# Performance work log

Measured on AMD Instinct MI355X. Metric: run time of the kernel, lower is better.

## Reference

```python
import jax, jax.numpy as jnp
import numpy as np

NUM_HEAD = 12
DIM_MODEL = 768
HEAD_DIM = DIM_MODEL // NUM_HEAD


def setup_inputs() -> dict:
    key = jax.random.key(0)
    ks = jax.random.split(key, 4)
    B, S, D = 2, 2048, DIM_MODEL
    scale = 1.0 / np.sqrt(D)
    return {
        "v1": jax.random.normal(ks[0], (B, S, D), dtype=jnp.float32),
        "v1_mask": jnp.zeros((B, 1, 1, S), dtype=jnp.float32),
        "Wq": jax.random.normal(ks[1], (D, D), dtype=jnp.float32) * scale,
        "bq": jnp.zeros((D,), dtype=jnp.float32),
        "Wk": jax.random.normal(ks[2], (D, D), dtype=jnp.float32) * scale,
        "bk": jnp.zeros((D,), dtype=jnp.float32),
        "Wv": jax.random.normal(ks[3], (D, D), dtype=jnp.float32) * scale,
        "bv": jnp.zeros((D,), dtype=jnp.float32),
    }


def reference(v1, v1_mask, Wq, bq, Wk, bk, Wv, bv):
    B, S, D = v1.shape
    H, hd = NUM_HEAD, HEAD_DIM

    def split_heads(x):  # [B,S,D] -> [B,H,S,hd]
        return x.reshape(B, S, H, hd).transpose(0, 2, 1, 3)

    q = split_heads(v1 @ Wq + bq)
    k = split_heads(v1 @ Wk + bk)
    v = split_heads(v1 @ Wv + bv)

    scores = jnp.einsum("bhqd,bhkd->bhqk", q, k) / jnp.sqrt(jnp.float32(hd))
    scores = scores + v1_mask  # additive mask broadcasts over heads/query
    probs = jax.nn.softmax(scores, axis=-1)
    # dropout is identity in eval/reference mode
    ctx = jnp.einsum("bhqk,bhkd->bhqd", probs, v)
    return ctx.transpose(0, 2, 1, 3).reshape(B, S, D)
```

## Files before the change

kernel.cpp:

```cpp
#include <hip/hip_runtime.h>
#include <math.h>

#define B_SZ 2
#define S_SZ 2048
#define D_SZ 768
#define NH   12
#define HD   64
#define BH_T (B_SZ * NH)
#define M_TOT (B_SZ * S_SZ)

using bfrag = __attribute__((ext_vector_type(8))) short;
using ffrag = __attribute__((ext_vector_type(4))) float;

__device__ __forceinline__ unsigned short f2bf(float f) {
    unsigned int u = __float_as_uint(f);
    u += 0x7fffu + ((u >> 16) & 1u);
    return (unsigned short)(u >> 16);
}
__device__ __forceinline__ unsigned short f2bf_fast(float f) {
    return (unsigned short)((__float_as_uint(f) + 0x8000u) >> 16);
}

__device__ __forceinline__ void async16(void* lds, const void* gp) {
    __builtin_amdgcn_global_load_lds(
        (const __attribute__((address_space(1))) unsigned int*)gp,
        (__attribute__((address_space(3))) unsigned int*)lds,
        16, 0, 0);
}

__global__ __launch_bounds__(256) void cvt_v1(const float* __restrict__ in,
                                              unsigned short* __restrict__ out) {
    int i = (blockIdx.x * 256 + threadIdx.x) * 4;
    float4 v = *(const float4*)&in[i];
    ushort4 o;
    o.x = f2bf(v.x); o.y = f2bf(v.y); o.z = f2bf(v.z); o.w = f2bf(v.w);
    *(ushort4*)&out[i] = o;
}

__global__ __launch_bounds__(256) void transpose_w(
    const float* __restrict__ Wq, const float* __restrict__ Wk,
    const float* __restrict__ Wv, unsigned short* __restrict__ Wt) {
    const int z = blockIdx.z;
    const float* W = (z == 0) ? Wq : (z == 1) ? Wk : Wv;
    unsigned short* dst = Wt + (size_t)z * D_SZ * D_SZ;
    __shared__ float tile[64][65];
    const int t = threadIdx.x;
    const int n0 = blockIdx.x * 64, k0 = blockIdx.y * 64;
    #pragma unroll
    for (int i = 0; i < 16; ++i) {
        int flat = i * 256 + t;
        int r = flat >> 6, c = flat & 63;
        tile[r][c] = W[(size_t)(k0 + r) * D_SZ + n0 + c];
    }
    __syncthreads();
    #pragma unroll
    for (int i = 0; i < 16; ++i) {
        int flat = i * 256 + t;
        int r = flat >> 6, c = flat & 63;
        dst[(size_t)(n0 + r) * D_SZ + k0 + c] = f2bf(tile[c][r]);
    }
}

__global__ __launch_bounds__(256) void proj_gemm(
    const unsigned short* __restrict__ Ab,
    const unsigned short* __restrict__ Wt,
    const float* __restrict__ bq, const float* __restrict__ bk_,
    const float* __restrict__ bv_,
    unsigned short* __restrict__ Qb, unsigned short* __restrict__ Kb,
    unsigned short* __restrict__ Vtb) {
    const int z = blockIdx.z;
    const unsigned short* Bt = Wt + (size_t)z * D_SZ * D_SZ;
    const float* bias = (z == 0) ? bq : (z == 1) ? bk_ : bv_;

    __shared__ unsigned short As[128 * 64];
    __shared__ unsigned short Bs[128 * 64];

    const int t = threadIdx.x;
    const int lane = t & 63;
    const int w = t >> 6;
    const int wm = w & 1, wn = w >> 1;
    const int col = lane & 15;
    const int quad = lane >> 4;
    const int m0 = blockIdx.y * 128;
    const int n0 = blockIdx.x * 128;
    const int wbase = t & ~63;

    ffrag acc[4][4];
    #pragma unroll
    for (int i = 0; i < 4; ++i)
        #pragma unroll
        for (int j = 0; j < 4; ++j) { ffrag zf = {0.f, 0.f, 0.f, 0.f}; acc[i][j] = zf; }

    for (int k0 = 0; k0 < D_SZ; k0 += 64) {
        __syncthreads();
        #pragma unroll
        for (int i = 0; i < 4; ++i) {
            int c = i * 256 + t;
            int row = c >> 3;
            int gcol = ((c & 7) ^ (row & 7)) * 8;
            async16(&As[(size_t)(i * 256 + wbase) * 8],
                    &Ab[(size_t)(m0 + row) * D_SZ + k0 + gcol]);
        }
        #pragma unroll
        for (int i = 0; i < 4; ++i) {
            int c = i * 256 + t;
            int row = c >> 3;
            int gcol = ((c & 7) ^ (row & 7)) * 8;
            async16(&Bs[(size_t)(i * 256 + wbase) * 8],
                    &Bt[(size_t)(n0 + row) * D_SZ + k0 + gcol]);
        }
        __syncthreads();
        #pragma unroll
        for (int kk = 0; kk < 64; kk += 32) {
            const int cc = (kk >> 3) + quad;
            bfrag a[4], b[4];
            #pragma unroll
            for (int mi = 0; mi < 4; ++mi) {
                int row = wm * 64 + mi * 16 + col;
                a[mi] = *(const bfrag*)&As[row * 64 + ((cc ^ (row & 7)) * 8)];
            }
            #pragma unroll
            for (int ni = 0; ni < 4; ++ni) {
                int row = wn * 64 + ni * 16 + col;
                b[ni] = *(const bfrag*)&Bs[row * 64 + ((cc ^ (row & 7)) * 8)];
            }
            if (z == 2) {
                #pragma unroll
                for (int mi = 0; mi < 4; ++mi)
                    #pragma unroll
                    for (int ni = 0; ni < 4; ++ni)
                        acc[mi][ni] = __builtin_amdgcn_mfma_f32_16x16x32_bf16(
                            a[mi], b[ni], acc[mi][ni], 0, 0, 0);
            } else {
                #pragma unroll
                for (int mi = 0; mi < 4; ++mi)
                    #pragma unroll
                    for (int ni = 0; ni < 4; ++ni)
                        acc[mi][ni] = __builtin_amdgcn_mfma_f32_16x16x32_bf16(
                            b[ni], a[mi], acc[mi][ni], 0, 0, 0);
            }
        }
    }

    if (z < 2) {
        unsigned short* Out = (z == 0) ? Qb : Kb;
        const float sc = (z == 0) ? 0.125f : 1.0f;
        #pragma unroll
        for (int mi = 0; mi < 4; ++mi) {
            int m = m0 + wm * 64 + mi * 16 + col;
            int bb = m >> 11, s = m & 2047;
            #pragma unroll
            for (int ni = 0; ni < 4; ++ni) {
                int nb = n0 + wn * 64 + ni * 16 + quad * 4;
                int h = nb >> 6, d = nb & 63;
                float4 b4 = *(const float4*)&bias[nb];
                float v0 = (acc[mi][ni][0] + b4.x) * sc;
                float v1 = (acc[mi][ni][1] + b4.y) * sc;
                float v2 = (acc[mi][ni][2] + b4.z) * sc;
                float v3 = (acc[mi][ni][3] + b4.w) * sc;
                uint2 pk;
                pk.x = (unsigned)f2bf(v0) | ((unsigned)f2bf(v1) << 16);
                pk.y = (unsigned)f2bf(v2) | ((unsigned)f2bf(v3) << 16);
                *(uint2*)&Out[(((size_t)(bb * NH + h)) * S_SZ + s) * HD + d] = pk;
            }
        }
    } else {
        #pragma unroll
        for (int ni = 0; ni < 4; ++ni) {
            int n = n0 + wn * 64 + ni * 16 + col;
            int h = n >> 6, d = n & 63;
            float bvv = bias[n];
            #pragma unroll
            for (int mi = 0; mi < 4; ++mi) {
                int mb = m0 + wm * 64 + mi * 16 + quad * 4;
                int bb = mb >> 11, s = mb & 2047;
                uint2 pk;
                pk.x = (unsigned)f2bf(acc[mi][ni][0] + bvv) |
                       ((unsigned)f2bf(acc[mi][ni][1] + bvv) << 16);
                pk.y = (unsigned)f2bf(acc[mi][ni][2] + bvv) |
                       ((unsigned)f2bf(acc[mi][ni][3] + bvv) << 16);
                *(uint2*)&Vtb[(((size_t)(bb * NH + h)) * HD + d) * S_SZ + s] = pk;
            }
        }
    }
}

__global__ __launch_bounds__(256) void attn_mfma(
    const unsigned short* __restrict__ Qb, const unsigned short* __restrict__ Kb,
    const unsigned short* __restrict__ Vt, const float* __restrict__ mask,
    float* __restrict__ out) {
    __shared__ unsigned short Qs[64 * 64];
    __shared__ unsigned short Ks[128 * 64];
    __shared__ unsigned short Vs[64 * 128];
    __shared__ unsigned short Ps[4][16 * 64];

    const int t = threadIdx.x;
    const int lane = t & 63;
    const int w = t >> 6;
    const int col = lane & 15;
    const int quad = lane >> 4;
    const int q0 = blockIdx.x * 64;
    const int bh = blockIdx.y;
    const int b = bh / NH, h = bh % NH;
    const int wbase = t & ~63;

    const unsigned short* Qg = Qb + (size_t)bh * S_SZ * HD;
    const unsigned short* Kg = Kb + (size_t)bh * S_SZ * HD;
    const unsigned short* Vg = Vt + (size_t)bh * S_SZ * HD;
    const float* mrow = mask + (size_t)b * S_SZ;

    #pragma unroll
    for (int i = 0; i < 2; ++i) {
        int c = i * 256 + t;
        int row = c >> 3;
        int gcol = ((c & 7) ^ (row & 7)) * 8;
        async16(&Qs[(size_t)(i * 256 + wbase) * 8],
                &Qg[(size_t)(q0 + row) * HD + gcol]);
    }

    ffrag o[4];
    #pragma unroll
    for (int i = 0; i < 4; ++i) { ffrag zf = {0.f, 0.f, 0.f, 0.f}; o[i] = zf; }
    float lsum[4] = {0.f, 0.f, 0.f, 0.f};

    for (int k0 = 0; k0 < S_SZ; k0 += 128) {
        __syncthreads();
        #pragma unroll
        for (int i = 0; i < 4; ++i) {
            int c = i * 256 + t;
            int row = c >> 3;
            int gcol = ((c & 7) ^ (row & 7)) * 8;
            async16(&Ks[(size_t)(i * 256 + wbase) * 8],
                    &Kg[(size_t)(k0 + row) * HD + gcol]);
        }
        #pragma unroll
        for (int i = 0; i < 4; ++i) {
            int c = i * 256 + t;
            int row = c >> 4;
            int cp = c & 15;
            int gch = (cp & 8) | ((cp ^ row) & 7);
            async16(&Vs[(size_t)(i * 256 + wbase) * 8],
                    &Vg[(size_t)row * S_SZ + k0 + gch * 8]);
        }
        __syncthreads();

        ffrag s[8];
        #pragma unroll
        for (int i = 0; i < 8; ++i) { ffrag zf = {0.f, 0.f, 0.f, 0.f}; s[i] = zf; }
        #pragma unroll
        for (int kk = 0; kk < 2; ++kk) {
            const int cc = kk * 4 + quad;
            const int arow = w * 16 + col;
            bfrag aq = *(const bfrag*)&Qs[arow * 64 + ((cc ^ (arow & 7)) * 8)];
            #pragma unroll
            for (int ni = 0; ni < 8; ++ni) {
                int brow = ni * 16 + col;
                bfrag bk8 = *(const bfrag*)&Ks[brow * 64 + ((cc ^ (brow & 7)) * 8)];
                s[ni] = __builtin_amdgcn_mfma_f32_16x16x32_bf16(aq, bk8, s[ni], 0, 0, 0);
            }
        }

        #pragma unroll
        for (int ni = 0; ni < 8; ++ni) {
            float mv = mrow[k0 + ni * 16 + col];
            #pragma unroll
            for (int r = 0; r < 4; ++r) {
                float e = __expf(s[ni][r] + mv);
                s[ni][r] = e;
                lsum[r] += e;
            }
        }

        unsigned short* Pw = &Ps[w][0];
        #pragma unroll
        for (int half = 0; half < 2; ++half) {
            #pragma unroll
            for (int ni = 0; ni < 4; ++ni) {
                #pragma unroll
                for (int r = 0; r < 4; ++r) {
                    int prow = quad * 4 + r;
                    int pcol = ni * 16 + col;
                    Pw[prow * 64 + (((pcol >> 3) ^ (prow & 7)) * 8) + (pcol & 7)] =
                        f2bf_fast(s[half * 4 + ni][r]);
                }
            }
            #pragma unroll
            for (int kk = 0; kk < 2; ++kk) {
                const int cc = kk * 4 + quad;
                const int prow = col;
                bfrag ap = *(const bfrag*)&Pw[prow * 64 + ((cc ^ (prow & 7)) * 8)];
                #pragma unroll
                for (int di = 0; di < 4; ++di) {
                    int vrow = di * 16 + col;
                    int ch = half * 8 + kk * 4 + quad;
                    bfrag bv8 = *(const bfrag*)
                        &Vs[vrow * 128 + ((ch & 8) | ((ch ^ vrow) & 7)) * 8];
                    o[di] = __builtin_amdgcn_mfma_f32_16x16x32_bf16(ap, bv8, o[di], 0, 0, 0);
                }
            }
        }
    }

    #pragma unroll
    for (int r = 0; r < 4; ++r) {
        #pragma unroll
        for (int off = 1; off < 16; off <<= 1)
            lsum[r] += __shfl_xor(lsum[r], off);
    }
    float inv[4];
    #pragma unroll
    for (int r = 0; r < 4; ++r) inv[r] = 1.0f / lsum[r];
    #pragma unroll
    for (int di = 0; di < 4; ++di) {
        int d = di * 16 + col;
        #pragma unroll
        for (int r = 0; r < 4; ++r) {
            int q = q0 + w * 16 + quad * 4 + r;
            out[((size_t)(b * S_SZ + q)) * D_SZ + h * HD + d] = o[di][r] * inv[r];
        }
    }
}

extern "C" void kernel_launch(void* const* d_in, const int* in_sizes, int n_in,
                              void* d_out, int out_size, void* d_ws, size_t ws_size,
                              hipStream_t stream) {
    const float* v1   = (const float*)d_in[0];
    const float* mask = (const float*)d_in[1];
    const float* Wq   = (const float*)d_in[2];
    const float* bq   = (const float*)d_in[3];
    const float* Wk   = (const float*)d_in[4];
    const float* bk   = (const float*)d_in[5];
    const float* Wv   = (const float*)d_in[6];
    const float* bv   = (const float*)d_in[7];
    float* out = (float*)d_out;

    unsigned short* ws = (unsigned short*)d_ws;
    const size_t per = (size_t)BH_T * S_SZ * HD;
    unsigned short* Qb  = ws;
    unsigned short* Kb  = Qb + per;
    unsigned short* Vtb = Kb + per;
    unsigned short* v1b = Vtb + per;
    unsigned short* Wt  = v1b + (size_t)M_TOT * D_SZ;

    cvt_v1<<<dim3((M_TOT * D_SZ) / 1024), 256, 0, stream>>>(v1, v1b);
    transpose_w<<<dim3(12, 12, 3), 256, 0, stream>>>(Wq, Wk, Wv, Wt);
    proj_gemm<<<dim3(6, 32, 3), 256, 0, stream>>>(v1b, Wt, bq, bk, bv, Qb, Kb, Vtb);
    attn_mfma<<<dim3(32, 24), 256, 0, stream>>>(Qb, Kb, Vtb, mask, out);
}
```

Measured before the change: 173.5 us.

## Split attention over key halves, stage projection epilogue through LDS

The attention kernel now splits the key range into two halves across a third grid dimension, doubling the block count from 768 to 1536. Each half writes unnormalized partial outputs and row sums, and a new combine kernel adds and normalizes them. The key tile shrinks to 64, Q fragments are held in registers, and the mask is staged in LDS. The projection GEMM epilogue now stages results through padded shared memory so global stores are 16-byte and coalesced, at the cost of extra partial-output traffic and an additional launch.

```diff
diff --git a/kernel.cpp b/kernel.cpp
--- a/kernel.cpp
+++ b/kernel.cpp
@@ -60,6 +60,8 @@
         dst[(size_t)(n0 + r) * D_SZ + k0 + c] = f2bf(tile[c][r]);
     }
 }
+
+#define CP_LD 136
 
 __global__ __launch_bounds__(256) void proj_gemm(
     const unsigned short* __restrict__ Ab,
@@ -72,8 +74,9 @@
     const unsigned short* Bt = Wt + (size_t)z * D_SZ * D_SZ;
     const float* bias = (z == 0) ? bq : (z == 1) ? bk_ : bv_;
 
-    __shared__ unsigned short As[128 * 64];
-    __shared__ unsigned short Bs[128 * 64];
+    __shared__ unsigned short smem[128 * CP_LD];
+    unsigned short* As = smem;
+    unsigned short* Bs = smem + 128 * 64;
 
     const int t = threadIdx.x;
     const int lane = t & 63;
@@ -142,45 +145,67 @@
         }
     }
 
+    __syncthreads();
+
     if (z < 2) {
+        const float sc = (z == 0) ? 0.125f : 1.0f;
+        #pragma unroll
+        for (int mi = 0; mi < 4; ++mi) {
+            int m_local = wm * 64 + mi * 16 + col;
+            #pragma unroll
+            for (int ni = 0; ni < 4; ++ni) {
+                int n_base = wn * 64 + ni * 16 + quad * 4;
+                float4 b4 = *(const float4*)&bias[n0 + n_base];
+                uint2 pk;
+                pk.x = (unsigned)f2bf((acc[mi][ni][0] + b4.x) * sc) |
+                       ((unsigned)f2bf((acc[mi][ni][1] + b4.y) * sc) << 16);
+                pk.y = (unsigned)f2bf((acc[mi][ni][2] + b4.z) * sc) |
+                       ((unsigned)f2bf((acc[mi][ni][3] + b4.w) * sc) << 16);
+                *(uint2*)&smem[m_local * CP_LD + n_base] = pk;
+            }
+        }
+        __syncthreads();
         unsigned short* Out = (z == 0) ? Qb : Kb;
-        const float sc = (z == 0) ? 0.125f : 1.0f;
-        #pragma unroll
-        for (int mi = 0; mi < 4; ++mi) {
-            int m = m0 + wm * 64 + mi * 16 + col;
+        #pragma unroll
+        for (int j = 0; j < 8; ++j) {
+            int flat = j * 256 + t;
+            int row = flat >> 4;
+            int ch = flat & 15;
+            uint4 vv = *(const uint4*)&smem[row * CP_LD + ch * 8];
+            int m = m0 + row;
             int bb = m >> 11, s = m & 2047;
-            #pragma unroll
-            for (int ni = 0; ni < 4; ++ni) {
-                int nb = n0 + wn * 64 + ni * 16 + quad * 4;
-                int h = nb >> 6, d = nb & 63;
-                float4 b4 = *(const float4*)&bias[nb];
-                float v0 = (acc[mi][ni][0] + b4.x) * sc;
-                float v1 = (acc[mi][ni][1] + b4.y) * sc;
-                float v2 = (acc[mi][ni][2] + b4.z) * sc;
-                float v3 = (acc[mi][ni][3] + b4.w) * sc;
-                uint2 pk;
-                pk.x = (unsigned)f2bf(v0) | ((unsigned)f2bf(v1) << 16);
-                pk.y = (unsigned)f2bf(v2) | ((unsigned)f2bf(v3) << 16);
-                *(uint2*)&Out[(((size_t)(bb * NH + h)) * S_SZ + s) * HD + d] = pk;
-            }
+            int h = (n0 >> 6) + (ch >> 3);
+            int d = (ch & 7) * 8;
+            *(uint4*)&Out[((size_t)(bb * NH + h) * S_SZ + s) * HD + d] = vv;
         }
     } else {
         #pragma unroll
         for (int ni = 0; ni < 4; ++ni) {
-            int n = n0 + wn * 64 + ni * 16 + col;
-            int h = n >> 6, d = n & 63;
-            float bvv = bias[n];
+            int n_local = wn * 64 + ni * 16 + col;
+            float bvv = bias[n0 + n_local];
             #pragma unroll
             for (int mi = 0; mi < 4; ++mi) {
-                int mb = m0 + wm * 64 + mi * 16 + quad * 4;
-                int bb = mb >> 11, s = mb & 2047;
+                int m_base = wm * 64 + mi * 16 + quad * 4;
                 uint2 pk;
                 pk.x = (unsigned)f2bf(acc[mi][ni][0] + bvv) |
                        ((unsigned)f2bf(acc[mi][ni][1] + bvv) << 16);
                 pk.y = (unsigned)f2bf(acc[mi][ni][2] + bvv) |
                        ((unsigned)f2bf(acc[mi][ni][3] + bvv) << 16);
-                *(uint2*)&Vtb[(((size_t)(bb * NH + h)) * HD + d) * S_SZ + s] = pk;
-            }
+                *(uint2*)&smem[n_local * CP_LD + m_base] = pk;
+            }
+        }
+        __syncthreads();
+        #pragma unroll
+        for (int j = 0; j < 8; ++j) {
+            int flat = j * 256 + t;
+            int row = flat >> 4;
+            int ch = flat & 15;
+            uint4 vv = *(const uint4*)&smem[row * CP_LD + ch * 8];
+            int n = n0 + row;
+            int h = n >> 6, d = n & 63;
+            int m = m0 + ch * 8;
+            int bb = m >> 11, s = m & 2047;
+            *(uint4*)&Vtb[((size_t)(bb * NH + h) * HD + d) * S_SZ + s] = vv;
         }
     }
 }
@@ -188,11 +213,11 @@
 __global__ __launch_bounds__(256) void attn_mfma(
     const unsigned short* __restrict__ Qb, const unsigned short* __restrict__ Kb,
     const unsigned short* __restrict__ Vt, const float* __restrict__ mask,
-    float* __restrict__ out) {
-    __shared__ unsigned short Qs[64 * 64];
-    __shared__ unsigned short Ks[128 * 64];
-    __shared__ unsigned short Vs[64 * 128];
+    float* __restrict__ O0, float* __restrict__ O1, float* __restrict__ lp) {
+    __shared__ unsigned short Ks[64 * 64];
+    __shared__ unsigned short Vs[64 * 64];
     __shared__ unsigned short Ps[4][16 * 64];
+    __shared__ float ms[64];
 
     const int t = threadIdx.x;
     const int lane = t & 63;
@@ -201,6 +226,7 @@
     const int quad = lane >> 4;
     const int q0 = blockIdx.x * 64;
     const int bh = blockIdx.y;
+    const int split = blockIdx.z;
     const int b = bh / NH, h = bh % NH;
     const int wbase = t & ~63;
 
@@ -214,8 +240,16 @@
         int c = i * 256 + t;
         int row = c >> 3;
         int gcol = ((c & 7) ^ (row & 7)) * 8;
-        async16(&Qs[(size_t)(i * 256 + wbase) * 8],
+        async16(&Ks[(size_t)(i * 256 + wbase) * 8],
                 &Qg[(size_t)(q0 + row) * HD + gcol]);
+    }
+    __syncthreads();
+    const int arow = w * 16 + col;
+    bfrag aq[2];
+    #pragma unroll
+    for (int kk = 0; kk < 2; ++kk) {
+        int cc = kk * 4 + quad;
+        aq[kk] = *(const bfrag*)&Ks[arow * 64 + ((cc ^ (arow & 7)) * 8)];
     }
 
     ffrag o[4];
@@ -223,46 +257,39 @@
     for (int i = 0; i < 4; ++i) { ffrag zf = {0.f, 0.f, 0.f, 0.f}; o[i] = zf; }
     float lsum[4] = {0.f, 0.f, 0.f, 0.f};
 
-    for (int k0 = 0; k0 < S_SZ; k0 += 128) {
-        __syncthreads();
-        #pragma unroll
-        for (int i = 0; i < 4; ++i) {
+    const int kbeg = split * (S_SZ / 2);
+    for (int k0 = kbeg; k0 < kbeg + S_SZ / 2; k0 += 64) {
+        __syncthreads();
+        #pragma unroll
+        for (int i = 0; i < 2; ++i) {
             int c = i * 256 + t;
             int row = c >> 3;
             int gcol = ((c & 7) ^ (row & 7)) * 8;
             async16(&Ks[(size_t)(i * 256 + wbase) * 8],
                     &Kg[(size_t)(k0 + row) * HD + gcol]);
-        }
-        #pragma unroll
-        for (int i = 0; i < 4; ++i) {
-            int c = i * 256 + t;
-            int row = c >> 4;
-            int cp = c & 15;
-            int gch = (cp & 8) | ((cp ^ row) & 7);
             async16(&Vs[(size_t)(i * 256 + wbase) * 8],
-                    &Vg[(size_t)row * S_SZ + k0 + gch * 8]);
-        }
-        __syncthreads();
-
-        ffrag s[8];
-        #pragma unroll
-        for (int i = 0; i < 8; ++i) { ffrag zf = {0.f, 0.f, 0.f, 0.f}; s[i] = zf; }
+                    &Vg[(size_t)row * S_SZ + k0 + gcol]);
+        }
+        if (t < 16) async16(&ms[0], &mrow[k0 + t * 4]);
+        __syncthreads();
+
+        ffrag s[4];
+        #pragma unroll
+        for (int i = 0; i < 4; ++i) { ffrag zf = {0.f, 0.f, 0.f, 0.f}; s[i] = zf; }
         #pragma unroll
         for (int kk = 0; kk < 2; ++kk) {
             const int cc = kk * 4 + quad;
-            const int arow = w * 16 + col;
-            bfrag aq = *(const bfrag*)&Qs[arow * 64 + ((cc ^ (arow & 7)) * 8)];
-            #pragma unroll
-            for (int ni = 0; ni < 8; ++ni) {
+            #pragma unroll
+            for (int ni = 0; ni < 4; ++ni) {
                 int brow = ni * 16 + col;
                 bfrag bk8 = *(const bfrag*)&Ks[brow * 64 + ((cc ^ (brow & 7)) * 8)];
-                s[ni] = __builtin_amdgcn_mfma_f32_16x16x32_bf16(aq, bk8, s[ni], 0, 0, 0);
-            }
-        }
-
-        #pragma unroll
-        for (int ni = 0; ni < 8; ++ni) {
-            float mv = mrow[k0 + ni * 16 + col];
+                s[ni] = __builtin_amdgcn_mfma_f32_16x16x32_bf16(aq[kk], bk8, s[ni], 0, 0, 0);
+            }
+        }
+
+        #pragma unroll
+        for (int ni = 0; ni < 4; ++ni) {
+            float mv = ms[ni * 16 + col];
             #pragma unroll
             for (int r = 0; r < 4; ++r) {
                 float e = __expf(s[ni][r] + mv);
@@ -273,30 +300,24 @@
 
         unsigned short* Pw = &Ps[w][0];
         #pragma unroll
-        for (int half = 0; half < 2; ++half) {
-            #pragma unroll
-            for (int ni = 0; ni < 4; ++ni) {
-                #pragma unroll
-                for (int r = 0; r < 4; ++r) {
-                    int prow = quad * 4 + r;
-                    int pcol = ni * 16 + col;
-                    Pw[prow * 64 + (((pcol >> 3) ^ (prow & 7)) * 8) + (pcol & 7)] =
-                        f2bf_fast(s[half * 4 + ni][r]);
-                }
-            }
-            #pragma unroll
-            for (int kk = 0; kk < 2; ++kk) {
-                const int cc = kk * 4 + quad;
-                const int prow = col;
-                bfrag ap = *(const bfrag*)&Pw[prow * 64 + ((cc ^ (prow & 7)) * 8)];
-                #pragma unroll
-                for (int di = 0; di < 4; ++di) {
-                    int vrow = di * 16 + col;
-                    int ch = half * 8 + kk * 4 + quad;
-                    bfrag bv8 = *(const bfrag*)
-                        &Vs[vrow * 128 + ((ch & 8) | ((ch ^ vrow) & 7)) * 8];
-                    o[di] = __builtin_amdgcn_mfma_f32_16x16x32_bf16(ap, bv8, o[di], 0, 0, 0);
-                }
+        for (int ni = 0; ni < 4; ++ni) {
+            #pragma unroll
+            for (int r = 0; r < 4; ++r) {
+                int prow = quad * 4 + r;
+                int pcol = ni * 16 + col;
+                Pw[prow * 64 + (((pcol >> 3) ^ (prow & 7)) * 8) + (pcol & 7)] =
+                    f2bf_fast(s[ni][r]);
+            }
+        }
+        #pragma unroll
+        for (int kk = 0; kk < 2; ++kk) {
+            const int cc = kk * 4 + quad;
+            bfrag ap = *(const bfrag*)&Pw[col * 64 + ((cc ^ (col & 7)) * 8)];
+            #pragma unroll
+            for (int di = 0; di < 4; ++di) {
+                int vrow = di * 16 + col;
+                bfrag bv8 = *(const bfrag*)&Vs[vrow * 64 + ((cc ^ (vrow & 7)) * 8)];
+                o[di] = __builtin_amdgcn_mfma_f32_16x16x32_bf16(ap, bv8, o[di], 0, 0, 0);
             }
         }
     }
@@ -307,18 +328,47 @@
         for (int off = 1; off < 16; off <<= 1)
             lsum[r] += __shfl_xor(lsum[r], off);
     }
-    float inv[4];
-    #pragma unroll
-    for (int r = 0; r < 4; ++r) inv[r] = 1.0f / lsum[r];
+
+    float* Optr = (split == 0) ? O0 : O1;
     #pragma unroll
     for (int di = 0; di < 4; ++di) {
         int d = di * 16 + col;
         #pragma unroll
         for (int r = 0; r < 4; ++r) {
             int q = q0 + w * 16 + quad * 4 + r;
-            out[((size_t)(b * S_SZ + q)) * D_SZ + h * HD + d] = o[di][r] * inv[r];
-        }
-    }
+            Optr[((size_t)(b * S_SZ + q)) * D_SZ + h * HD + d] = o[di][r];
+        }
+    }
+    if (col == 0) {
+        #pragma unroll
+        for (int r = 0; r < 4; ++r) {
+            int q = q0 + w * 16 + quad * 4 + r;
+            lp[((size_t)(split * B_SZ + b) * NH + h) * S_SZ + q] = lsum[r];
+        }
+    }
+}
+
+__global__ __launch_bounds__(256) void combine(
+    float* __restrict__ out, const float* __restrict__ O1,
+    const float* __restrict__ lp) {
+    int i4 = blockIdx.x * 256 + threadIdx.x;
+    int flat = i4 * 4;
+    int b = flat / (S_SZ * D_SZ);
+    int rem = flat % (S_SZ * D_SZ);
+    int q = rem / D_SZ;
+    int c = rem % D_SZ;
+    int h = c >> 6;
+    size_t l0i = ((size_t)b * NH + h) * S_SZ + q;
+    float l = lp[l0i] + lp[(size_t)B_SZ * NH * S_SZ + l0i];
+    float inv = 1.0f / l;
+    float4 a = *(const float4*)&out[flat];
+    float4 p = *(const float4*)&O1[flat];
+    float4 r;
+    r.x = (a.x + p.x) * inv;
+    r.y = (a.y + p.y) * inv;
+    r.z = (a.z + p.z) * inv;
+    r.w = (a.w + p.w) * inv;
+    *(float4*)&out[flat] = r;
 }
 
 extern "C" void kernel_launch(void* const* d_in, const int* in_sizes, int n_in,
@@ -334,16 +384,19 @@
     const float* bv   = (const float*)d_in[7];
     float* out = (float*)d_out;
 
-    unsigned short* ws = (unsigned short*)d_ws;
-    const size_t per = (size_t)BH_T * S_SZ * HD;
-    unsigned short* Qb  = ws;
-    unsigned short* Kb  = Qb + per;
-    unsigned short* Vtb = Kb + per;
-    unsigned short* v1b = Vtb + per;
-    unsigned short* Wt  = v1b + (size_t)M_TOT * D_SZ;
+    char* ws = (char*)d_ws;
+    const size_t per_b = (size_t)BH_T * S_SZ * HD * 2;
+    unsigned short* Qb  = (unsigned short*)(ws);
+    unsigned short* Kb  = (unsigned short*)(ws + per_b);
+    unsigned short* Vtb = (unsigned short*)(ws + 2 * per_b);
+    unsigned short* v1b = (unsigned short*)(ws + 3 * per_b);
+    unsigned short* Wt  = (unsigned short*)(ws + 3 * per_b + (size_t)M_TOT * D_SZ * 2);
+    float* O1 = (float*)(ws + 3 * per_b);
+    float* lp = (float*)(ws + 3 * per_b + (size_t)M_TOT * D_SZ * 4);
 
     cvt_v1<<<dim3((M_TOT * D_SZ) / 1024), 256, 0, stream>>>(v1, v1b);
     transpose_w<<<dim3(12, 12, 3), 256, 0, stream>>>(Wq, Wk, Wv, Wt);
     proj_gemm<<<dim3(6, 32, 3), 256, 0, stream>>>(v1b, Wt, bq, bk, bv, Qb, Kb, Vtb);
-    attn_mfma<<<dim3(32, 24), 256, 0, stream>>>(Qb, Kb, Vtb, mask, out);
-}
+    attn_mfma<<<dim3(32, 24, 2), 256, 0, stream>>>(Qb, Kb, Vtb, mask, out, O1, lp);
+    combine<<<dim3((M_TOT * D_SZ) / 1024), 256, 0, stream>>>(out, O1, lp);
+}
```

Measured after the change: 168.4 us. 2.9% less time.
